# Kernel tuning notes

Measured on AMD Instinct MI355X. Metric: run time of the kernel, lower is better.

The kernel has to match this reference:

```python
import jax, jax.numpy as jnp
import numpy as np

N_HEADS = 16
NEG_FILL = -1000000000.0  # masked_fill value from the torch module
PADDING = 0.0             # default padding arg


def setup_inputs() -> dict:
    key = jax.random.key(0)
    kq, kk, kv = jax.random.split(key, 3)
    B, S, D = 2, 2048, 1024
    q = jax.random.normal(kq, (B, S, D), dtype=jnp.float32)
    k = jax.random.normal(kk, (B, S, D), dtype=jnp.float32)
    v = jax.random.normal(kv, (B, S, D), dtype=jnp.float32)
    return {"q": q, "k": k, "v": v, "is_masked": 1}


def reference(q, k, v, is_masked):
    B, S, D = q.shape
    d_key = D // N_HEADS

    def split_heads(x):  # [B,S,D] -> [B,H,S,d_key]
        return x.reshape(B, S, N_HEADS, d_key).transpose(0, 2, 1, 3)

    qh, kh, vh = split_heads(q), split_heads(k), split_heads(v)
    scale = 1.0 / jnp.sqrt(jnp.asarray(d_key, dtype=q.dtype))
    # [B,H,S,S] raw attention scores
    scores = jnp.einsum("bhqd,bhkd->bhqk", qh, kh) * scale
    # value-based mask: keep positions where score != padding
    mask = scores != PADDING
    if is_masked:
        causal = jnp.tril(jnp.ones((S, S), dtype=bool))  # [S,S]
        mask = mask & causal
    scores = jnp.where(mask, scores, jnp.asarray(NEG_FILL, dtype=scores.dtype))
    probs = jax.nn.softmax(scores, axis=-1)
    out = jnp.einsum("bhqk,bhkd->bhqd", probs, vh)  # [B,H,S,d_key]
    return out.transpose(0, 2, 1, 3).reshape(B, S, D)
```

## Files before the change

kernel.cpp:

```cpp
#include <hip/hip_runtime.h>
#include <hip/hip_bf16.h>
#include <math.h>
#include <type_traits>

typedef __bf16 bf16x8 __attribute__((ext_vector_type(8)));
typedef float f32x4 __attribute__((ext_vector_type(4)));

#define S_LEN 2048
#define D_MODEL 1024
#define LT 72
#define CEXP 0.18033688011112042f

__device__ __forceinline__ float fast_exp2(float x) {
    return __builtin_amdgcn_exp2f(x);
}

template<bool BF>
__device__ __forceinline__ void body(
    const void* __restrict__ qv, const void* __restrict__ kv,
    const void* __restrict__ vv, void* __restrict__ outv,
    int maskflag, int z, int bh,
    __bf16* Ks0, __bf16* Ks1, __bf16* Vt0, __bf16* Vt1, __bf16* Ps)
{
    const int b    = bh >> 4;
    const int h    = bh & 15;
    const int t    = threadIdx.x;
    const int w    = t >> 6;
    const int lane = t & 63;
    const int m16  = lane & 15;
    const int quad = lane >> 4;

    const int q0 = z * 64;
    const size_t head_off = (size_t)b * S_LEN * D_MODEL + (size_t)h * 64;

    const __bf16* qb = (const __bf16*)qv; const float* qf = (const float*)qv;
    const __bf16* kb = (const __bf16*)kv; const float* kf = (const float*)kv;
    const __bf16* vb = (const __bf16*)vv; const float* vf = (const float*)vv;

    bf16x8 aq0, aq1;
    {
        const int r = q0 + w * 16 + m16;
        if (BF) {
            const __bf16* p = qb + head_off + (size_t)r * D_MODEL;
            aq0 = *(const bf16x8*)&p[quad * 8];
            aq1 = *(const bf16x8*)&p[32 + quad * 8];
        } else {
            const float* p = qf + head_off + (size_t)r * D_MODEL;
            #pragma unroll
            for (int half = 0; half < 2; ++half) {
                float4 x0 = *(const float4*)&p[half * 32 + quad * 8];
                float4 x1 = *(const float4*)&p[half * 32 + quad * 8 + 4];
                bf16x8 f = { (__bf16)x0.x, (__bf16)x0.y, (__bf16)x0.z, (__bf16)x0.w,
                             (__bf16)x1.x, (__bf16)x1.y, (__bf16)x1.z, (__bf16)x1.w };
                if (half == 0) aq0 = f; else aq1 = f;
            }
        }
    }

    f32x4 o[4];
    #pragma unroll
    for (int i = 0; i < 4; ++i) o[i] = (f32x4){0.f,0.f,0.f,0.f};
    float lsum = 0.f;

    const int kg = t >> 4, dg = t & 15;
    const int k0 = kg * 4, d0 = dg * 4;
    const int cst = k0 ^ ((dg & 7) << 3);

    const int ktmax = maskflag ? z : (S_LEN / 64 - 1);

    float4 kr[4], vr[4];
    auto pref = [&](int kt) {
        if (BF) {
            const __bf16* base = kb + head_off + (size_t)kt * 64 * D_MODEL;
            #pragma unroll
            for (int i = 0; i < 2; ++i) {
                int c = t + i * 256, row = c >> 3, off = (c & 7) << 3;
                *(uint4*)&kr[i] = *(const uint4*)&base[(size_t)row * D_MODEL + off];
            }
            const __bf16* vp = vb + head_off + (size_t)(kt * 64 + k0) * D_MODEL + d0;
            #pragma unroll
            for (int j = 0; j < 4; ++j)
                *(uint2*)&vr[j] = *(const uint2*)&vp[(size_t)j * D_MODEL];
        } else {
            const float* base = kf + head_off + (size_t)kt * 64 * D_MODEL;
            #pragma unroll
            for (int i = 0; i < 4; ++i) {
                int c = t + i * 256, row = c >> 4, off = (c & 15) << 2;
                kr[i] = *(const float4*)&base[(size_t)row * D_MODEL + off];
            }
            const float* vp = vf + head_off + (size_t)(kt * 64 + k0) * D_MODEL + d0;
            #pragma unroll
            for (int j = 0; j < 4; ++j)
                vr[j] = *(const float4*)&vp[(size_t)j * D_MODEL];
        }
    };
    auto stage = [&](__bf16* Ks, __bf16* Vt) {
        if (BF) {
            #pragma unroll
            for (int i = 0; i < 2; ++i) {
                int c = t + i * 256, row = c >> 3, off = (c & 7) << 3;
                *(uint4*)&Ks[row * LT + off] = *(const uint4*)&kr[i];
            }
            union { uint2 u; __bf16 hh[4]; } r[4];
            #pragma unroll
            for (int j = 0; j < 4; ++j) r[j].u = *(const uint2*)&vr[j];
            #pragma unroll
            for (int j = 0; j < 4; ++j) {
                __bf16 pk[4] = { r[0].hh[j], r[1].hh[j], r[2].hh[j], r[3].hh[j] };
                *(uint2*)&Vt[(d0 + j) * LT + cst] = *(uint2*)pk;
            }
        } else {
            #pragma unroll
            for (int i = 0; i < 4; ++i) {
                int c = t + i * 256, row = c >> 4, off = (c & 15) << 2;
                float4 ld = kr[i];
                __bf16 pk[4] = { (__bf16)ld.x, (__bf16)ld.y, (__bf16)ld.z, (__bf16)ld.w };
                *(uint2*)&Ks[row * LT + off] = *(uint2*)pk;
            }
            #pragma unroll
            for (int j = 0; j < 4; ++j) {
                __bf16 pk[4] = { (__bf16)vr[0][j], (__bf16)vr[1][j],
                                 (__bf16)vr[2][j], (__bf16)vr[3][j] };
                *(uint2*)&Vt[(d0 + j) * LT + cst] = *(uint2*)pk;
            }
        }
    };

    pref(0);
    for (int kt = 0; kt <= ktmax; ++kt) {
        __bf16* Ks = (kt & 1) ? Ks1 : Ks0;
        __bf16* Vt = (kt & 1) ? Vt1 : Vt0;
        stage(Ks, Vt);
        __syncthreads();
        if (kt < ktmax) pref(kt + 1);

        bf16x8 bk0[4], bk1[4], bv0[4], bv1[4];
        #pragma unroll
        for (int nt = 0; nt < 4; ++nt) {
            bk0[nt] = *(bf16x8*)&Ks[(nt * 16 + m16) * LT + quad * 8];
            bk1[nt] = *(bf16x8*)&Ks[(nt * 16 + m16) * LT + 32 + quad * 8];
        }
        #pragma unroll
        for (int dt = 0; dt < 4; ++dt) {
            int dim = dt * 16 + m16;
            int sw = ((dim >> 2) & 7) << 3;
            bv0[dt] = *(bf16x8*)&Vt[dim * LT + ((quad * 8) ^ sw)];
            bv1[dt] = *(bf16x8*)&Vt[dim * LT + ((quad * 8 + 32) ^ sw)];
        }

        f32x4 s[4];
        #pragma unroll
        for (int nt = 0; nt < 4; ++nt) {
            f32x4 acc = (f32x4){0.f,0.f,0.f,0.f};
            acc = __builtin_amdgcn_mfma_f32_16x16x32_bf16(bk0[nt], aq0, acc, 0, 0, 0);
            acc = __builtin_amdgcn_mfma_f32_16x16x32_bf16(bk1[nt], aq1, acc, 0, 0, 0);
            s[nt] = acc;
        }

        const bool diag = maskflag && (kt == z);
        const int qloc = w * 16 + m16;
        #pragma unroll
        for (int nt = 0; nt < 4; ++nt) {
            union { uint2 u; __bf16 hh[4]; } pk;
            #pragma unroll
            for (int reg = 0; reg < 4; ++reg) {
                float raw = s[nt][reg];
                bool valid = (raw != 0.0f);
                if (diag) valid = valid && ((nt * 16 + quad * 4 + reg) <= qloc);
                float p = valid ? fast_exp2(raw * CEXP) : 0.0f;
                lsum += p;
                pk.hh[reg] = (__bf16)p;
            }
            *(uint2*)&Ps[(w * 16 + m16) * LT + nt * 16 + quad * 4] = pk.u;
        }

        bf16x8 ap0 = *(bf16x8*)&Ps[(w * 16 + m16) * LT + quad * 8];
        bf16x8 ap1 = *(bf16x8*)&Ps[(w * 16 + m16) * LT + 32 + quad * 8];
        #pragma unroll
        for (int dt = 0; dt < 4; ++dt) {
            o[dt] = __builtin_amdgcn_mfma_f32_16x16x32_bf16(ap0, bv0[dt], o[dt], 0, 0, 0);
            o[dt] = __builtin_amdgcn_mfma_f32_16x16x32_bf16(ap1, bv1[dt], o[dt], 0, 0, 0);
        }
    }

    float l = lsum;
    l += __shfl_xor(l, 16, 64);
    l += __shfl_xor(l, 32, 64);
    #pragma unroll
    for (int reg = 0; reg < 4; ++reg) {
        float li = __shfl(l, quad * 4 + reg, 64);
        float invl = 1.0f / li;
        int srow = q0 + w * 16 + quad * 4 + reg;
        #pragma unroll
        for (int dt = 0; dt < 4; ++dt) {
            size_t idx = head_off + (size_t)srow * D_MODEL + dt * 16 + m16;
            float val = o[dt][reg] * invl;
            if (BF) ((__bf16*)outv)[idx] = (__bf16)val;
            else    ((float*)outv)[idx]  = val;
        }
    }
}

__global__ __launch_bounds__(256, 3)
void mha_flash_kernel(const void* __restrict__ qv,
                      const void* __restrict__ kv,
                      const void* __restrict__ vv,
                      const int* __restrict__ is_masked_p,
                      void* __restrict__ outv)
{
    __shared__ __attribute__((aligned(16))) __bf16 Ks0[64 * LT];
    __shared__ __attribute__((aligned(16))) __bf16 Ks1[64 * LT];
    __shared__ __attribute__((aligned(16))) __bf16 Vt0[64 * LT];
    __shared__ __attribute__((aligned(16))) __bf16 Vt1[64 * LT];
    __shared__ __attribute__((aligned(16))) __bf16 Ps [64 * LT];

    const int id  = blockIdx.x;
    const int xcd = id & 7;
    const int r   = id >> 3;
    const int z   = 31 - (r >> 2);
    const int bh  = xcd * 4 + (r & 3);

    const int maskflag = *is_masked_p;

    const __bf16* qprobe = (const __bf16*)qv;
    float px = (float)qprobe[2 * (threadIdx.x & 63)];
    bool okp = (px == px) && (fabsf(px) > 1e-6f) && (fabsf(px) < 100.0f);
    unsigned long long bal = __ballot(okp);
    const bool isbf16 = (__popcll(bal) >= 48);

    if (isbf16)
        body<true >(qv, kv, vv, outv, maskflag, z, bh, Ks0, Ks1, Vt0, Vt1, Ps);
    else
        body<false>(qv, kv, vv, outv, maskflag, z, bh, Ks0, Ks1, Vt0, Vt1, Ps);
}

extern "C" void kernel_launch(void* const* d_in, const int* in_sizes, int n_in,
                              void* d_out, int out_size, void* d_ws, size_t ws_size,
                              hipStream_t stream) {
    const int* is_masked = (const int*)d_in[3];
    mha_flash_kernel<<<dim3(1024), 256, 0, stream>>>(d_in[0], d_in[1], d_in[2], is_masked, d_out);
}
```

Before: 126.6 us.

## Process two 64-row query groups per block to reuse K/V tiles

Each block now handles 128 query rows as two 64-row groups that share every staged K/V tile, halving the grid to 512 blocks and halving K/V global loads and LDS staging per query. The first group skips tiles beyond its causal range, and the block-to-tile mapping pairs a long and a short causal range for load balance. MFMA sections are wrapped in s_setprio, and launch bounds drop to 2 blocks per CU to make room for the doubled accumulators. The cost is higher register pressure, lower occupancy, and fewer blocks to spread across the CUs.

Result: slower. 140.5 us (+11.0%).

```diff
diff --git a/kernel.cpp b/kernel.cpp
--- a/kernel.cpp
+++ b/kernel.cpp
@@ -1,7 +1,6 @@
 #include <hip/hip_runtime.h>
 #include <hip/hip_bf16.h>
 #include <math.h>
-#include <type_traits>
 
 typedef __bf16 bf16x8 __attribute__((ext_vector_type(8)));
 typedef float f32x4 __attribute__((ext_vector_type(4)));
@@ -30,43 +29,46 @@
     const int m16  = lane & 15;
     const int quad = lane >> 4;
 
-    const int q0 = z * 64;
+    const int q0 = z * 128;
     const size_t head_off = (size_t)b * S_LEN * D_MODEL + (size_t)h * 64;
 
     const __bf16* qb = (const __bf16*)qv; const float* qf = (const float*)qv;
     const __bf16* kb = (const __bf16*)kv; const float* kf = (const float*)kv;
     const __bf16* vb = (const __bf16*)vv; const float* vf = (const float*)vv;
 
-    bf16x8 aq0, aq1;
-    {
-        const int r = q0 + w * 16 + m16;
+    bf16x8 aq0[2], aq1[2];
+    #pragma unroll
+    for (int g = 0; g < 2; ++g) {
+        const int r = q0 + g * 64 + w * 16 + m16;
         if (BF) {
             const __bf16* p = qb + head_off + (size_t)r * D_MODEL;
-            aq0 = *(const bf16x8*)&p[quad * 8];
-            aq1 = *(const bf16x8*)&p[32 + quad * 8];
+            aq0[g] = *(const bf16x8*)&p[quad * 8];
+            aq1[g] = *(const bf16x8*)&p[32 + quad * 8];
         } else {
             const float* p = qf + head_off + (size_t)r * D_MODEL;
             #pragma unroll
             for (int half = 0; half < 2; ++half) {
                 float4 x0 = *(const float4*)&p[half * 32 + quad * 8];
                 float4 x1 = *(const float4*)&p[half * 32 + quad * 8 + 4];
-                bf16x8 f = { (__bf16)x0.x, (__bf16)x0.y, (__bf16)x0.z, (__bf16)x0.w,
-                             (__bf16)x1.x, (__bf16)x1.y, (__bf16)x1.z, (__bf16)x1.w };
-                if (half == 0) aq0 = f; else aq1 = f;
+                bf16x8 fr = { (__bf16)x0.x, (__bf16)x0.y, (__bf16)x0.z, (__bf16)x0.w,
+                              (__bf16)x1.x, (__bf16)x1.y, (__bf16)x1.z, (__bf16)x1.w };
+                if (half == 0) aq0[g] = fr; else aq1[g] = fr;
             }
         }
     }
 
-    f32x4 o[4];
+    f32x4 o[2][4];
     #pragma unroll
-    for (int i = 0; i < 4; ++i) o[i] = (f32x4){0.f,0.f,0.f,0.f};
-    float lsum = 0.f;
+    for (int g = 0; g < 2; ++g)
+        #pragma unroll
+        for (int i = 0; i < 4; ++i) o[g][i] = (f32x4){0.f,0.f,0.f,0.f};
+    float lsum[2] = {0.f, 0.f};
 
     const int kg = t >> 4, dg = t & 15;
     const int k0 = kg * 4, d0 = dg * 4;
     const int cst = k0 ^ ((dg & 7) << 3);
 
-    const int ktmax = maskflag ? z : (S_LEN / 64 - 1);
+    const int ktmax = maskflag ? (2 * z + 1) : (S_LEN / 64 - 1);
 
     float4 kr[4], vr[4];
     auto pref = [&](int kt) {
@@ -125,6 +127,9 @@
             }
         }
     };
+
+    const int qloc = w * 16 + m16;
+    const int prow = (w * 16 + m16) * LT;
 
     pref(0);
     for (int kt = 0; kt <= ktmax; ++kt) {
@@ -134,6 +139,10 @@
         __syncthreads();
         if (kt < ktmax) pref(kt + 1);
 
+        const bool act0  = !(maskflag && kt > 2 * z);
+        const bool diag0 = maskflag && (kt == 2 * z);
+        const bool diag1 = maskflag && (kt == 2 * z + 1);
+
         bf16x8 bk0[4], bk1[4], bv0[4], bv1[4];
         #pragma unroll
         for (int nt = 0; nt < 4; ++nt) {
@@ -148,60 +157,113 @@
             bv1[dt] = *(bf16x8*)&Vt[dim * LT + ((quad * 8 + 32) ^ sw)];
         }
 
-        f32x4 s[4];
+        f32x4 s0[4], s1[4];
+        __builtin_amdgcn_s_setprio(1);
+        if (act0) {
+            #pragma unroll
+            for (int nt = 0; nt < 4; ++nt) {
+                f32x4 acc = (f32x4){0.f,0.f,0.f,0.f};
+                acc = __builtin_amdgcn_mfma_f32_16x16x32_bf16(bk0[nt], aq0[0], acc, 0, 0, 0);
+                acc = __builtin_amdgcn_mfma_f32_16x16x32_bf16(bk1[nt], aq1[0], acc, 0, 0, 0);
+                s0[nt] = acc;
+            }
+        }
         #pragma unroll
         for (int nt = 0; nt < 4; ++nt) {
             f32x4 acc = (f32x4){0.f,0.f,0.f,0.f};
-            acc = __builtin_amdgcn_mfma_f32_16x16x32_bf16(bk0[nt], aq0, acc, 0, 0, 0);
-            acc = __builtin_amdgcn_mfma_f32_16x16x32_bf16(bk1[nt], aq1, acc, 0, 0, 0);
-            s[nt] = acc;
-        }
-
-        const bool diag = maskflag && (kt == z);
-        const int qloc = w * 16 + m16;
+            acc = __builtin_amdgcn_mfma_f32_16x16x32_bf16(bk0[nt], aq0[1], acc, 0, 0, 0);
+            acc = __builtin_amdgcn_mfma_f32_16x16x32_bf16(bk1[nt], aq1[1], acc, 0, 0, 0);
+            s1[nt] = acc;
+        }
+        __builtin_amdgcn_s_setprio(0);
+
+        bf16x8 ap00, ap01;
+        if (act0) {
+            #pragma unroll
+            for (int nt = 0; nt < 4; ++nt) {
+                union { uint2 u; __bf16 hh[4]; } pk;
+                float ps[4];
+                #pragma unroll
+                for (int reg = 0; reg < 4; ++reg) {
+                    float raw = s0[nt][reg];
+                    bool valid = (raw != 0.0f);
+                    if (diag0) valid = valid && ((nt * 16 + quad * 4 + reg) <= qloc);
+                    float p = valid ? fast_exp2(raw * CEXP) : 0.0f;
+                    ps[reg] = p;
+                    pk.hh[reg] = (__bf16)p;
+                }
+                lsum[0] += (ps[0] + ps[1]) + (ps[2] + ps[3]);
+                *(uint2*)&Ps[prow + nt * 16 + quad * 4] = pk.u;
+            }
+            ap00 = *(bf16x8*)&Ps[prow + quad * 8];
+            ap01 = *(bf16x8*)&Ps[prow + 32 + quad * 8];
+        }
+
+        uint2 pk1s[4];
         #pragma unroll
         for (int nt = 0; nt < 4; ++nt) {
             union { uint2 u; __bf16 hh[4]; } pk;
+            float ps[4];
             #pragma unroll
             for (int reg = 0; reg < 4; ++reg) {
-                float raw = s[nt][reg];
+                float raw = s1[nt][reg];
                 bool valid = (raw != 0.0f);
-                if (diag) valid = valid && ((nt * 16 + quad * 4 + reg) <= qloc);
+                if (diag1) valid = valid && ((nt * 16 + quad * 4 + reg) <= qloc);
                 float p = valid ? fast_exp2(raw * CEXP) : 0.0f;
-                lsum += p;
+                ps[reg] = p;
                 pk.hh[reg] = (__bf16)p;
             }
-            *(uint2*)&Ps[(w * 16 + m16) * LT + nt * 16 + quad * 4] = pk.u;
-        }
-
-        bf16x8 ap0 = *(bf16x8*)&Ps[(w * 16 + m16) * LT + quad * 8];
-        bf16x8 ap1 = *(bf16x8*)&Ps[(w * 16 + m16) * LT + 32 + quad * 8];
+            lsum[1] += (ps[0] + ps[1]) + (ps[2] + ps[3]);
+            pk1s[nt] = pk.u;
+        }
+
+        if (act0) {
+            __builtin_amdgcn_s_setprio(1);
+            #pragma unroll
+            for (int dt = 0; dt < 4; ++dt) {
+                o[0][dt] = __builtin_amdgcn_mfma_f32_16x16x32_bf16(ap00, bv0[dt], o[0][dt], 0, 0, 0);
+                o[0][dt] = __builtin_amdgcn_mfma_f32_16x16x32_bf16(ap01, bv1[dt], o[0][dt], 0, 0, 0);
+            }
+            __builtin_amdgcn_s_setprio(0);
+        }
+
+        #pragma unroll
+        for (int nt = 0; nt < 4; ++nt)
+            *(uint2*)&Ps[prow + nt * 16 + quad * 4] = pk1s[nt];
+        bf16x8 ap10 = *(bf16x8*)&Ps[prow + quad * 8];
+        bf16x8 ap11 = *(bf16x8*)&Ps[prow + 32 + quad * 8];
+
+        __builtin_amdgcn_s_setprio(1);
         #pragma unroll
         for (int dt = 0; dt < 4; ++dt) {
-            o[dt] = __builtin_amdgcn_mfma_f32_16x16x32_bf16(ap0, bv0[dt], o[dt], 0, 0, 0);
-            o[dt] = __builtin_amdgcn_mfma_f32_16x16x32_bf16(ap1, bv1[dt], o[dt], 0, 0, 0);
-        }
+            o[1][dt] = __builtin_amdgcn_mfma_f32_16x16x32_bf16(ap10, bv0[dt], o[1][dt], 0, 0, 0);
+            o[1][dt] = __builtin_amdgcn_mfma_f32_16x16x32_bf16(ap11, bv1[dt], o[1][dt], 0, 0, 0);
+        }
+        __builtin_amdgcn_s_setprio(0);
     }
 
-    float l = lsum;
-    l += __shfl_xor(l, 16, 64);
-    l += __shfl_xor(l, 32, 64);
     #pragma unroll
-    for (int reg = 0; reg < 4; ++reg) {
-        float li = __shfl(l, quad * 4 + reg, 64);
-        float invl = 1.0f / li;
-        int srow = q0 + w * 16 + quad * 4 + reg;
-        #pragma unroll
-        for (int dt = 0; dt < 4; ++dt) {
-            size_t idx = head_off + (size_t)srow * D_MODEL + dt * 16 + m16;
-            float val = o[dt][reg] * invl;
-            if (BF) ((__bf16*)outv)[idx] = (__bf16)val;
-            else    ((float*)outv)[idx]  = val;
+    for (int g = 0; g < 2; ++g) {
+        float l = lsum[g];
+        l += __shfl_xor(l, 16, 64);
+        l += __shfl_xor(l, 32, 64);
+        #pragma unroll
+        for (int reg = 0; reg < 4; ++reg) {
+            float li = __shfl(l, quad * 4 + reg, 64);
+            float invl = 1.0f / li;
+            int srow = q0 + g * 64 + w * 16 + quad * 4 + reg;
+            #pragma unroll
+            for (int dt = 0; dt < 4; ++dt) {
+                size_t idx = head_off + (size_t)srow * D_MODEL + dt * 16 + m16;
+                float val = o[g][dt][reg] * invl;
+                if (BF) ((__bf16*)outv)[idx] = (__bf16)val;
+                else    ((float*)outv)[idx]  = val;
+            }
         }
     }
 }
 
-__global__ __launch_bounds__(256, 3)
+__global__ __launch_bounds__(256, 2)
 void mha_flash_kernel(const void* __restrict__ qv,
                       const void* __restrict__ kv,
                       const void* __restrict__ vv,
@@ -214,11 +276,14 @@
     __shared__ __attribute__((aligned(16))) __bf16 Vt1[64 * LT];
     __shared__ __attribute__((aligned(16))) __bf16 Ps [64 * LT];
 
-    const int id  = blockIdx.x;
-    const int xcd = id & 7;
-    const int r   = id >> 3;
-    const int z   = 31 - (r >> 2);
-    const int bh  = xcd * 4 + (r & 3);
+    const int id   = blockIdx.x;
+    const int xcd  = id & 7;
+    const int idx  = id >> 3;
+    const int f    = idx & 31;
+    const int s2   = idx >> 5;
+    const int bh   = xcd * 4 + (f >> 3);
+    const int zsl  = f & 7;
+    const int z    = s2 ? zsl : (15 - zsl);
 
     const int maskflag = *is_masked_p;
 
@@ -238,5 +303,5 @@
                               void* d_out, int out_size, void* d_ws, size_t ws_size,
                               hipStream_t stream) {
     const int* is_masked = (const int*)d_in[3];
-    mha_flash_kernel<<<dim3(1024), 256, 0, stream>>>(d_in[0], d_in[1], d_in[2], is_masked, d_out);
+    mha_flash_kernel<<<dim3(512), 256, 0, stream>>>(d_in[0], d_in[1], d_in[2], is_masked, d_out);
 }
```
